# Optimization experiments

Hardware: AMD Instinct MI355X
Metric: run time of the kernel (lower is better)

Reference implementation:

```python
import jax, jax.numpy as jnp
import numpy as np
from jax import lax

T_LOW, T_HIGH = 100.0, 200.0   # init kwargs of Canny
TG22 = 0.4142135623730951      # tan(22.5 deg), cv2's direction quantization constant
MAX_ITERS = 512                # safety cap on hysteresis fixed-point loop


def _shift(a, dy, dx):
    # neighbor value n[y, x] = a[y + dy, x + dx], zero outside
    H, W = a.shape
    p = jnp.pad(a, 1)
    return p[1 + dy:1 + dy + H, 1 + dx:1 + dx + W]


def _canny(x):
    B, C, H, W = x.shape
    # toRGB: ((x+1)/2*255).to(uint8)  (truncation; values are non-negative)
    img = jnp.clip(jnp.floor((x + 1.0) * 0.5 * 255.0), 0.0, 255.0)
    # original reshapes batch into one tall strip (B*H, W, C) before cv2.Canny
    img = img.transpose(0, 2, 3, 1).reshape(B * H, W, C)
    HH = B * H
    p = jnp.pad(img, ((1, 1), (1, 1), (0, 0)), mode='edge')  # replicate border like cv2

    def s(dy, dx):
        return p[1 + dy:1 + dy + HH, 1 + dx:1 + dx + W, :]

    # 3x3 Sobel per channel
    gx = (s(-1, 1) + 2.0 * s(0, 1) + s(1, 1)) - (s(-1, -1) + 2.0 * s(0, -1) + s(1, -1))
    gy = (s(1, -1) + 2.0 * s(1, 0) + s(1, 1)) - (s(-1, -1) + 2.0 * s(-1, 0) + s(-1, 1))
    mag_c = jnp.abs(gx) + jnp.abs(gy)  # L1 magnitude (cv2 default L2gradient=False)
    # multi-channel: take channel with max magnitude per pixel (cv2 behavior)
    idx = jnp.argmax(mag_c, axis=-1, keepdims=True)
    gx = jnp.take_along_axis(gx, idx, -1)[..., 0]
    gy = jnp.take_along_axis(gy, idx, -1)[..., 0]
    mag = jnp.take_along_axis(mag_c, idx, -1)[..., 0]

    # non-maximum suppression with 4 quantized directions
    ax_, ay_ = jnp.abs(gx), jnp.abs(gy)
    is_h = ay_ < TG22 * ax_          # gradient ~horizontal -> compare left/right
    is_v = ay_ * TG22 > ax_          # gradient ~vertical -> compare up/down
    same = (gx * gy) >= 0.0          # diagonal orientation by sign agreement
    n1 = jnp.where(is_h, _shift(mag, 0, -1),
         jnp.where(is_v, _shift(mag, -1, 0),
         jnp.where(same, _shift(mag, -1, -1), _shift(mag, -1, 1))))
    n2 = jnp.where(is_h, _shift(mag, 0, 1),
         jnp.where(is_v, _shift(mag, 1, 0),
         jnp.where(same, _shift(mag, 1, 1), _shift(mag, 1, -1))))
    keep = (mag > n1) & (mag >= n2)

    strong = keep & (mag > T_HIGH)
    weak = keep & (mag > T_LOW)

    # hysteresis: propagate strong labels through 8-connected weak pixels to fixed point
    def dilate(m):
        mf = m.astype(jnp.float32)
        return lax.reduce_window(mf, 0.0, lax.add, (3, 3), (1, 1), 'SAME') > 0.0

    def body(st):
        s0, _, it = st
        grown = (dilate(s0) & weak) | s0
        return grown, jnp.any(grown != s0), it + 1

    def cond(st):
        return st[1] & (st[2] < MAX_ITERS)

    strong, _, _ = lax.while_loop(cond, body, (strong, jnp.array(True), jnp.array(0)))

    edges = strong.reshape(B, H, W).astype(jnp.float32)        # {0,1} == cv2 {0,255}/255
    edges = jnp.broadcast_to(edges[:, None, :, :], (B, 3, H, W))
    return (edges - 0.5) / 0.5                                 # T.Normalize(0.5, 0.5)


def setup_inputs() -> dict:
    key = jax.random.key(0)
    x = jax.random.uniform(key, (16, 3, 512, 512), jnp.float32, -1.0, 1.0)
    return {"x": x}


def reference(x):
    return _canny(x)
```

## Files before the change

### kernel.cpp

```cpp
#include <hip/hip_runtime.h>
#include <stdint.h>

#define HH 8192
#define WW 512
#define WPR 8
#define TG22F 0.4142135623730951f
#define NSWEEP 8


__device__ __forceinline__ float to_img(float v) {
    float t = floorf((v + 1.0f) * 0.5f * 255.0f);
    return fminf(fmaxf(t, 0.0f), 255.0f);
}

__device__ __forceinline__ int bsel(uint64_t w0, uint64_t w1, int idx) {
    return (idx < 8) ? (int)((w0 >> (idx * 8)) & 255)
                     : (int)((w1 >> ((idx - 8) * 8)) & 255);
}

__device__ __forceinline__ uint64_t runfill(uint64_t s, uint64_t w) {
    uint64_t sw = s & w;
    uint64_t up = ((sw + w) ^ w) & w;
    uint64_t rs = __brevll(sw);
    uint64_t rw = __brevll(w);
    uint64_t dn = __brevll(((rs + rw) ^ rw) & rw);
    return up | dn | sw;
}

__global__ void k_sobel(const float* __restrict__ in, uint16_t* __restrict__ packed) {
    __shared__ uint8_t simg[3 * 34 * 72];
    const int tid = threadIdx.x;
    const int row0 = (blockIdx.x >> 3) << 5;
    const int col0 = (blockIdx.x & 7) << 6;

    for (int i = tid; i < 1632; i += 256) {
        int c = i / 544;
        int rem = i - c * 544;
        int hr = rem >> 4;
        int q = rem & 15;
        int gy = row0 + hr - 1;
        gy = gy < 0 ? 0 : (gy >= HH ? HH - 1 : gy);
        int b = gy >> 9, h = gy & 511;
        const float4 v = *(const float4*)&in[((((b * 3 + c) << 9) + h) << 9) + col0 + (q << 2)];
        uint32_t pk = (uint32_t)(uint8_t)to_img(v.x)
                    | ((uint32_t)(uint8_t)to_img(v.y) << 8)
                    | ((uint32_t)(uint8_t)to_img(v.z) << 16)
                    | ((uint32_t)(uint8_t)to_img(v.w) << 24);
        *(uint32_t*)&simg[(c * 34 + hr) * 72 + 4 + (q << 2)] = pk;
    }
    for (int i = tid; i < 204; i += 256) {
        int c = i / 68;
        int rem = i - c * 68;
        int hr = rem >> 1;
        int side = rem & 1;
        int gy = row0 + hr - 1;
        gy = gy < 0 ? 0 : (gy >= HH ? HH - 1 : gy);
        int gc = side ? col0 + 64 : col0 - 1;
        gc = gc < 0 ? 0 : (gc >= WW ? WW - 1 : gc);
        int b = gy >> 9, h = gy & 511;
        float v = to_img(in[((((b * 3 + c) << 9) + h) << 9) + gc]);
        simg[(c * 34 + hr) * 72 + (side ? 68 : 3)] = (uint8_t)v;
    }
    __syncthreads();

    const int r = tid >> 3;
    const int c8 = (tid & 7) << 3;

    int bestMag[8], bgx[8], bgy[8];
    #pragma unroll
    for (int j = 0; j < 8; ++j) { bestMag[j] = -1; bgx[j] = 0; bgy[j] = 0; }

    #pragma unroll
    for (int c = 0; c < 3; ++c) {
        const uint8_t* base = &simg[(c * 34 + r) * 72 + c8];
        uint64_t w00 = *(const uint64_t*)(base);
        uint64_t w01 = *(const uint64_t*)(base + 8);
        uint64_t w10 = *(const uint64_t*)(base + 72);
        uint64_t w11 = *(const uint64_t*)(base + 80);
        uint64_t w20 = *(const uint64_t*)(base + 144);
        uint64_t w21 = *(const uint64_t*)(base + 152);
        int vs[10], t0[10], t2[10];
        #pragma unroll
        for (int i = 0; i < 10; ++i) {
            int a0 = bsel(w00, w01, 3 + i);
            int a1 = bsel(w10, w11, 3 + i);
            int a2 = bsel(w20, w21, 3 + i);
            vs[i] = a0 + 2 * a1 + a2;
            t0[i] = a0; t2[i] = a2;
        }
        #pragma unroll
        for (int j = 0; j < 8; ++j) {
            int gx = vs[j + 2] - vs[j];
            int gy = (t2[j] + 2 * t2[j + 1] + t2[j + 2]) - (t0[j] + 2 * t0[j + 1] + t0[j + 2]);
            int mg = abs(gx) + abs(gy);
            if (mg > bestMag[j]) { bestMag[j] = mg; bgx[j] = gx; bgy[j] = gy; }
        }
    }

    uint32_t res[4];
    #pragma unroll
    for (int jj = 0; jj < 4; ++jj) {
        uint32_t pair = 0;
        #pragma unroll
        for (int s = 0; s < 2; ++s) {
            int j = jj * 2 + s;
            float axf = (float)abs(bgx[j]);
            float ayf = (float)abs(bgy[j]);
            int dir;
            if (ayf < TG22F * axf)      dir = 0;
            else if (ayf * TG22F > axf) dir = 1;
            else                        dir = (bgx[j] * bgy[j] >= 0) ? 2 : 3;
            uint32_t val = (uint32_t)(bestMag[j] | (dir << 12));
            pair |= val << (s * 16);
        }
        res[jj] = pair;
    }
    int y = row0 + r;
    *(uint4*)&packed[y * WW + col0 + c8] = *(uint4*)res;
}

__global__ void k_nms(const uint16_t* __restrict__ packed,
                      unsigned long long* __restrict__ strongB,
                      unsigned long long* __restrict__ weakB) {
    int y = blockIdx.x >> 1;
    int x = ((blockIdx.x & 1) << 8) + threadIdx.x;
    uint16_t own = packed[y * WW + x];
    int mag = own & 0xFFF;
    int dir = own >> 12;
    int d1y = (dir == 0) ? 0 : -1;
    int d1x = (dir == 0) ? -1 : (dir == 1) ? 0 : (dir == 2) ? -1 : 1;
    int n1y = y + d1y, n1x = x + d1x;
    int n2y = y - d1y, n2x = x - d1x;
    int n1 = (n1y >= 0 && n1y < HH && n1x >= 0 && n1x < WW) ? (packed[n1y * WW + n1x] & 0xFFF) : 0;
    int n2 = (n2y >= 0 && n2y < HH && n2x >= 0 && n2x < WW) ? (packed[n2y * WW + n2x] & 0xFFF) : 0;
    bool keep = (mag > n1) && (mag >= n2);
    bool strong = keep && (mag > 200);
    bool weak   = keep && (mag > 100);
    unsigned long long sb = __ballot(strong ? 1 : 0);
    unsigned long long wb = __ballot(weak ? 1 : 0);
    if ((threadIdx.x & 63) == 0) {
        int word = y * WPR + (x >> 6);
        strongB[word] = sb;
        weakB[word]   = wb;
    }
}

__global__ void k_sweep(const unsigned long long* __restrict__ weakB,
                        unsigned long long* __restrict__ buf) {
    __shared__ uint64_t tA[34][8];
    __shared__ uint64_t tB[34][8];
    const int tid = threadIdx.x;
    const int b = blockIdx.x;
    const int r = tid >> 3;
    const int k = tid & 7;
    const int gw = (b * 32 + r) * WPR + k;
    const uint64_t wk = weakB[gw];
    const uint64_t loaded = buf[gw];
    tA[r + 1][k] = loaded;
    if (tid < 8) {
        uint64_t h = (b > 0) ? buf[(b * 32 - 1) * WPR + tid] : 0ull;
        tA[0][tid] = h; tB[0][tid] = h;
    } else if (tid < 16) {
        int kk = tid - 8;
        uint64_t h = (b < 255) ? buf[(b * 32 + 32) * WPR + kk] : 0ull;
        tA[33][kk] = h; tB[33][kk] = h;
    }
    __syncthreads();

    uint64_t (*src)[8] = tA;
    uint64_t (*dst)[8] = tB;
    uint64_t own = loaded;
    for (int it = 0; it < 1024; ++it) {
        uint64_t acc = 0;
        #pragma unroll
        for (int dr = 0; dr < 3; ++dr) {
            uint64_t c = src[r + dr][k];
            uint64_t h = c | (c << 1) | (c >> 1);
            if (k > 0) h |= src[r + dr][k - 1] >> 63;
            if (k < 7) h |= src[r + dr][k + 1] << 63;
            acc |= h;
        }
        uint64_t nv = runfill(own | (acc & wk), wk);
        dst[r + 1][k] = nv;
        int any = __syncthreads_or((nv != own) ? 1 : 0);
        own = nv;
        uint64_t (*t)[8] = src; src = dst; dst = t;
        if (!any) break;
    }
    if (own != loaded) buf[gw] = own;
}

__global__ void k_out(const unsigned long long* __restrict__ result, float* __restrict__ out) {
    int t = blockIdx.x * blockDim.x + threadIdx.x;
    int b = t >> 16;
    int r = t & 65535;
    int h = r >> 7;
    int w = (r & 127) << 2;
    int y = (b << 9) + h;
    unsigned long long word = result[y * WPR + (w >> 6)];
    int sh = w & 63;
    float4 v;
    v.x = ((word >> (sh + 0)) & 1ull) ? 1.0f : -1.0f;
    v.y = ((word >> (sh + 1)) & 1ull) ? 1.0f : -1.0f;
    v.z = ((word >> (sh + 2)) & 1ull) ? 1.0f : -1.0f;
    v.w = ((word >> (sh + 3)) & 1ull) ? 1.0f : -1.0f;
    int base = (b * 3) << 18;
    int off = (h << 9) + w;
    *(float4*)&out[base + off] = v;
    *(float4*)&out[base + 262144 + off] = v;
    *(float4*)&out[base + 524288 + off] = v;
}

extern "C" void kernel_launch(void* const* d_in, const int* in_sizes, int n_in,
                              void* d_out, int out_size, void* d_ws, size_t ws_size,
                              hipStream_t stream) {
    const float* x = (const float*)d_in[0];
    float* out = (float*)d_out;
    char* ws = (char*)d_ws;

    uint16_t* packed          = (uint16_t*)(ws);
    unsigned long long* buf   = (unsigned long long*)(ws + 8388608);
    unsigned long long* weakB = (unsigned long long*)(ws + 8912896);

    k_sobel<<<2048, 256, 0, stream>>>(x, packed);
    k_nms<<<HH * 2, 256, 0, stream>>>(packed, buf, weakB);
    for (int s = 0; s < NSWEEP; ++s) {
        k_sweep<<<256, 256, 0, stream>>>(weakB, buf);
    }
    k_out<<<(HH * WW) / 1024, 256, 0, stream>>>(buf, out);
}
```

Baseline: 142.2 us.

## Early-exit converged hysteresis sweeps and enlarge sweep tiles to 64 rows

Each sweep block now covers 64 rows, two per thread, using 128 blocks instead of 256. A device flag array records whether any block changed the strong mask in a sweep, and later sweep launches return at once when the previous sweep changed nothing. The internal 1024-iteration cap is removed, so a block loops until its tile converges. This cuts the number of cross-block halo sweeps needed and skips redundant launches, at the cost of half as many blocks (less parallelism) and longer serial loops inside each block.

```diff
diff --git a/kernel.cpp b/kernel.cpp
--- a/kernel.cpp
+++ b/kernel.cpp
@@ -121,7 +121,9 @@
 
 __global__ void k_nms(const uint16_t* __restrict__ packed,
                       unsigned long long* __restrict__ strongB,
-                      unsigned long long* __restrict__ weakB) {
+                      unsigned long long* __restrict__ weakB,
+                      int* __restrict__ flags) {
+    if (blockIdx.x == 0 && threadIdx.x < 16) flags[threadIdx.x] = 0;
     int y = blockIdx.x >> 1;
     int x = ((blockIdx.x & 1) << 8) + threadIdx.x;
     uint16_t own = packed[y * WW + x];
@@ -145,49 +147,68 @@
     }
 }
 
-__global__ void k_sweep(const unsigned long long* __restrict__ weakB,
-                        unsigned long long* __restrict__ buf) {
-    __shared__ uint64_t tA[34][8];
-    __shared__ uint64_t tB[34][8];
+__global__ void __launch_bounds__(256) k_sweep(
+        const unsigned long long* __restrict__ weakB,
+        unsigned long long* __restrict__ buf,
+        int* __restrict__ flags, int sidx)
+{
+    if (sidx > 0 && flags[sidx - 1] == 0) return;
+    __shared__ uint64_t tA[66][8];
+    __shared__ uint64_t tB[66][8];
     const int tid = threadIdx.x;
     const int b = blockIdx.x;
     const int r = tid >> 3;
     const int k = tid & 7;
-    const int gw = (b * 32 + r) * WPR + k;
-    const uint64_t wk = weakB[gw];
-    const uint64_t loaded = buf[gw];
-    tA[r + 1][k] = loaded;
+    const int g0 = (b * 64 + r) * WPR + k;
+    const int g1 = g0 + 32 * WPR;
+    const uint64_t wk0 = weakB[g0];
+    const uint64_t wk1 = weakB[g1];
+    const uint64_t l0 = buf[g0];
+    const uint64_t l1 = buf[g1];
+    tA[r + 1][k]  = l0;
+    tA[r + 33][k] = l1;
     if (tid < 8) {
-        uint64_t h = (b > 0) ? buf[(b * 32 - 1) * WPR + tid] : 0ull;
+        uint64_t h = (b > 0) ? buf[(b * 64 - 1) * WPR + tid] : 0ull;
         tA[0][tid] = h; tB[0][tid] = h;
     } else if (tid < 16) {
         int kk = tid - 8;
-        uint64_t h = (b < 255) ? buf[(b * 32 + 32) * WPR + kk] : 0ull;
-        tA[33][kk] = h; tB[33][kk] = h;
+        uint64_t h = (b < 127) ? buf[(b * 64 + 64) * WPR + kk] : 0ull;
+        tA[65][kk] = h; tB[65][kk] = h;
     }
     __syncthreads();
 
     uint64_t (*src)[8] = tA;
     uint64_t (*dst)[8] = tB;
-    uint64_t own = loaded;
-    for (int it = 0; it < 1024; ++it) {
-        uint64_t acc = 0;
+    uint64_t o0 = l0, o1 = l1;
+    for (;;) {
+        uint64_t acc0 = 0, acc1 = 0;
         #pragma unroll
         for (int dr = 0; dr < 3; ++dr) {
-            uint64_t c = src[r + dr][k];
-            uint64_t h = c | (c << 1) | (c >> 1);
-            if (k > 0) h |= src[r + dr][k - 1] >> 63;
-            if (k < 7) h |= src[r + dr][k + 1] << 63;
-            acc |= h;
-        }
-        uint64_t nv = runfill(own | (acc & wk), wk);
-        dst[r + 1][k] = nv;
-        int any = __syncthreads_or((nv != own) ? 1 : 0);
-        own = nv;
+            uint64_t c0v = src[r + dr][k];
+            uint64_t h0 = c0v | (c0v << 1) | (c0v >> 1);
+            if (k > 0) h0 |= src[r + dr][k - 1] >> 63;
+            if (k < 7) h0 |= src[r + dr][k + 1] << 63;
+            acc0 |= h0;
+            uint64_t c1v = src[r + 32 + dr][k];
+            uint64_t h1 = c1v | (c1v << 1) | (c1v >> 1);
+            if (k > 0) h1 |= src[r + 32 + dr][k - 1] >> 63;
+            if (k < 7) h1 |= src[r + 32 + dr][k + 1] << 63;
+            acc1 |= h1;
+        }
+        uint64_t n0 = runfill(o0 | (acc0 & wk0), wk0);
+        uint64_t n1 = runfill(o1 | (acc1 & wk1), wk1);
+        dst[r + 1][k]  = n0;
+        dst[r + 33][k] = n1;
+        int any = __syncthreads_or((int)((n0 != o0) | (n1 != o1)));
+        o0 = n0; o1 = n1;
         uint64_t (*t)[8] = src; src = dst; dst = t;
         if (!any) break;
     }
-    if (own != loaded) buf[gw] = own;
+    bool ch = (o0 != l0) || (o1 != l1);
+    if (o0 != l0) buf[g0] = o0;
+    if (o1 != l1) buf[g1] = o1;
+    if (__ballot(ch ? 1 : 0) != 0ull && (tid & 63) == 0)
+        __hip_atomic_store(&flags[sidx], 1, __ATOMIC_RELAXED, __HIP_MEMORY_SCOPE_AGENT);
 }
 
 __global__ void k_out(const unsigned long long* __restrict__ result, float* __restrict__ out) {
@@ -221,11 +242,11 @@
     uint16_t* packed          = (uint16_t*)(ws);
     unsigned long long* buf   = (unsigned long long*)(ws + 8388608);
     unsigned long long* weakB = (unsigned long long*)(ws + 8912896);
+    int* flags                = (int*)(ws + 9437184);
 
     k_sobel<<<2048, 256, 0, stream>>>(x, packed);
-    k_nms<<<HH * 2, 256, 0, stream>>>(packed, buf, weakB);
-    for (int s = 0; s < NSWEEP; ++s) {
-        k_sweep<<<256, 256, 0, stream>>>(weakB, buf);
-    }
-    k_out<<<(HH * WW) / 1024, 256, 0, stream>>>(buf, out);
-}
+    k_nms<<<HH * 2, 256, 0, stream>>>(packed, buf, weakB, flags);
+    for (int s = 0; s < NSWEEP; ++s)
+        k_sweep<<<128, 256, 0, stream>>>(weakB, buf, flags, s);
+    k_out<<<4096, 256, 0, stream>>>(buf, out);
+}
```

Measured after the change: 139.9 us. No clear change (-1.7%).
